# Kernel tuning notes

Measured on AMD Instinct MI355X. Metric: run time of the kernel, lower is better.

The kernel has to match this reference:

```python
import jax, jax.numpy as jnp
import numpy as np

B, C, H, W = 2, 64, 64, 128
HW = H * W
PCR = (0.0, -25.6, -3.0, 51.2, 25.6, 1.0)  # point cloud range x/y/z min, x/y/z max
VOX = (0.1, 0.1, 4.0)                      # voxel size
NX = int(round((PCR[3] - PCR[0]) / VOX[0]))  # 512
NY = int(round((PCR[4] - PCR[1]) / VOX[1]))  # 512
BIG = 1e10  # masked-out distance (avoid inf for clean vjp)


def _rand_points(key):
    k_xyz, k_i = jax.random.split(key)
    u = jax.random.uniform(k_xyz, (B, 3, H, W), jnp.float32)
    lo = jnp.array([PCR[0], PCR[1], PCR[2]], jnp.float32).reshape(1, 3, 1, 1)
    hi = jnp.array([PCR[3], PCR[4], PCR[5]], jnp.float32).reshape(1, 3, 1, 1)
    xyz = lo + u * (hi - lo)
    inten = jax.random.uniform(k_i, (B, 1, H, W), jnp.float32)
    return jnp.concatenate([xyz, inten], axis=1)  # (B,4,H,W)


def setup_inputs() -> dict:
    key = jax.random.key(0)
    k1, k2, k3, k4, k5 = jax.random.split(key, 5)
    return {
        "fv_features": jax.random.normal(k1, (B, C, H, W), jnp.float32),
        "points_img": _rand_points(k2),
        "proj_masks": jax.random.randint(k4, (B, H, W), 0, 2).astype(jnp.int32),
        "points_img_far": _rand_points(k3),
        "proj_masks_far": jax.random.randint(k5, (B, H, W), 0, 2).astype(jnp.int32),
    }


def _three_interpolate(near_pts, near_feats, near_valid, far_pts):
    """pointnet2 three_nn + three_interpolate with invalid near points masked.
    near_pts: (N,3), near_feats: (N,C), near_valid: (N,) bool, far_pts: (M,3).
    Returns interpolated far features (M,C)."""
    # squared distances via |a|^2 + |b|^2 - 2 a.b  -> (M, N), avoids (M,N,3) temp
    d2 = (jnp.sum(far_pts * far_pts, -1)[:, None]
          + jnp.sum(near_pts * near_pts, -1)[None, :]
          - 2.0 * far_pts @ near_pts.T)
    d2 = jnp.where(near_valid[None, :], d2, BIG)
    neg_d, idx = jax.lax.top_k(-d2, 3)        # 3 nearest near-points per far point
    dist = -neg_d                              # squared dists, as in pointnet2 CUDA
    dist_recip = 1.0 / (dist + 1e-8)
    weight = dist_recip / jnp.sum(dist_recip, axis=-1, keepdims=True)  # (M,3)
    gathered = near_feats[idx]                 # (M,3,C)
    return jnp.einsum('mk,mkc->mc', weight, gathered)


def _scatter_bev(pts, feats, valid):
    """Mean-scatter point features into the BEV grid. pts:(N,3) feats:(N,C) valid:(N,)."""
    ix = jnp.floor((pts[:, 0] - PCR[0]) / VOX[0]).astype(jnp.int32)
    iy = jnp.floor((pts[:, 1] - PCR[1]) / VOX[1]).astype(jnp.int32)
    in_range = (ix >= 0) & (ix < NX) & (iy >= 0) & (iy < NY)
    w = (valid & in_range).astype(feats.dtype)            # zero-weight invalid pts
    flat = jnp.clip(iy, 0, NY - 1) * NX + jnp.clip(ix, 0, NX - 1)
    sums = jnp.zeros((NY * NX, feats.shape[1]), feats.dtype).at[flat].add(feats * w[:, None])
    cnt = jnp.zeros((NY * NX,), feats.dtype).at[flat].add(w)
    bev = sums / jnp.maximum(cnt, 1.0)[:, None]
    return bev.reshape(NY, NX, -1).transpose(2, 0, 1)      # (C, NY, NX)


def reference(fv_features, points_img, proj_masks, points_img_far, proj_masks_far):
    feats = fv_features.transpose(0, 2, 3, 1).reshape(B, HW, C)
    pts = points_img[:, :3].transpose(0, 2, 3, 1).reshape(B, HW, 3)
    pts_far = points_img_far[:, :3].transpose(0, 2, 3, 1).reshape(B, HW, 3)
    m = proj_masks.reshape(B, HW) > 0
    m_far = proj_masks_far.reshape(B, HW) > 0
    outs = []
    for k in range(B):  # small fixed batch loop, mirrors original per-sample loop
        interp = _three_interpolate(pts[k], feats[k], m[k], pts_far[k])
        all_pts = jnp.concatenate([pts[k], pts_far[k]], axis=0)
        all_feats = jnp.concatenate([feats[k], interp], axis=0)
        all_valid = jnp.concatenate([m[k], m_far[k]], axis=0)
        outs.append(_scatter_bev(all_pts, all_feats, all_valid))
    return jnp.stack(outs, axis=0)  # (B, C, NY, NX)
```

## Files before the change

kernel.cpp:

```cpp
#include <hip/hip_runtime.h>
#include <math.h>

constexpr int B_  = 2;
constexpr int C_  = 64;
constexpr int HW_ = 64 * 128;
constexpr int N_  = HW_;
constexpr int NX_ = 512;
constexpr int NY_ = 512;
constexpr int NYNX_ = NX_ * NY_;
constexpr int GC_  = 32;
constexpr int GCC_ = GC_ * GC_;
constexpr int CAP_ = 48;
constexpr int LPF_ = 8;
constexpr int BN_  = B_ * N_;
constexpr int NNB_ = BN_ / (256 / LPF_);

__device__ __forceinline__ int voxel_of(float x, float y, float w) {
#pragma clang fp contract(off)
  if (w == 0.0f) return -1;
  float qx = (x - 0.0f) / 0.1f;
  float qy = (y - (-25.6f)) / 0.1f;
  int ix = (int)floorf(qx);
  int iy = (int)floorf(qy);
  if (ix < 0 || ix >= NX_ || iy < 0 || iy >= NY_) return -1;
  return iy * NX_ + ix;
}

__device__ __forceinline__ int gcell_x(float x) {
  int c = (int)floorf(x * 0.625f);
  return min(GC_ - 1, max(0, c));
}
__device__ __forceinline__ int gcell_y(float y) {
  int c = (int)floorf((y + 25.6f) * 0.625f);
  return min(GC_ - 1, max(0, c));
}

__global__ __launch_bounds__(256) void prep_kernel(
    const float* __restrict__ fv,
    const float* __restrict__ pi, const int* __restrict__ pm,
    const float* __restrict__ pif, const int* __restrict__ pmf,
    float4* __restrict__ near4, float4* __restrict__ far4,
    float* __restrict__ cnt, int* __restrict__ gcellcnt,
    float4* __restrict__ gpts, int* __restrict__ gidx,
    float* __restrict__ acc, float* __restrict__ fvT) {
#pragma clang fp contract(off)
  __shared__ float tile[64][65];
  if (blockIdx.x < 64) {
    int t = blockIdx.x * 256 + threadIdx.x;
    int k = t / N_, n = t % N_;
    const float* base  = pi  + (size_t)k * 4 * HW_;
    const float* basef = pif + (size_t)k * 4 * HW_;
    float x = base[n], y = base[HW_ + n], z = base[2 * HW_ + n];
    bool v = pm[k * HW_ + n] > 0;
    near4[t] = make_float4(x, y, z, v ? 1.0f : 0.0f);
    float fx = basef[n], fy = basef[HW_ + n], fz = basef[2 * HW_ + n];
    bool vf = pmf[k * HW_ + n] > 0;
    far4[t] = make_float4(fx, fy, fz, vf ? 1.0f : 0.0f);

    if (v) {
      float sq = (x * x + y * y) + z * z;
      int c = gcell_y(y) * GC_ + gcell_x(x);
      int p = atomicAdd(&gcellcnt[k * GCC_ + c], 1);
      if (p < CAP_) {
        size_t o = (size_t)(k * GCC_ + c) * CAP_ + p;
        gpts[o] = make_float4(x, y, z, sq);
        gidx[o] = n;
      }
    }

    float4 z4 = make_float4(0.0f, 0.0f, 0.0f, 0.0f);
    int vn = voxel_of(x, y, v ? 1.0f : 0.0f);
    if (vn >= 0) {
      float old = atomicAdd(&cnt[(size_t)k * NYNX_ + vn], 1.0f);
      if (old == 1.0f) {
        float4* row = (float4*)(acc + ((size_t)k * NYNX_ + vn) * C_);
#pragma unroll
        for (int i = 0; i < C_ / 4; ++i) row[i] = z4;
      }
    }
    int vfv = voxel_of(fx, fy, vf ? 1.0f : 0.0f);
    if (vfv >= 0) {
      float old2 = atomicAdd(&cnt[(size_t)k * NYNX_ + vfv], 1.0f);
      if (old2 == 1.0f) {
        float4* row = (float4*)(acc + ((size_t)k * NYNX_ + vfv) * C_);
#pragma unroll
        for (int i = 0; i < C_ / 4; ++i) row[i] = z4;
      }
    }
  } else {
    int bid = blockIdx.x - 64;
    int k = bid >> 7;
    int n0 = (bid & 127) * 64;
    int tx = threadIdx.x & 63, ty = threadIdx.x >> 6;
    for (int c = ty; c < C_; c += 4)
      tile[c][tx] = fv[((size_t)(k * C_ + c)) * HW_ + n0 + tx];
    __syncthreads();
    for (int nn = ty; nn < 64; nn += 4)
      fvT[((size_t)(k * HW_ + n0 + nn)) * C_ + tx] = tile[tx][nn];
  }
}

__device__ __forceinline__ void merge3L(float tv, int idx,
                                        float& b0, float& b1, float& b2,
                                        int& i0, int& i1, int& i2) {
  bool w0 = (tv < b0) || (tv == b0 && idx < i0);
  bool w1 = (tv < b1) || (tv == b1 && idx < i1);
  bool w2 = (tv < b2) || (tv == b2 && idx < i2);
  float ob0 = b0, ob1 = b1;
  int   oi0 = i0, oi1 = i1;
  b0 = w0 ? tv : b0;                    i0 = w0 ? idx : i0;
  b1 = w0 ? ob0 : (w1 ? tv : b1);       i1 = w0 ? oi0 : (w1 ? idx : i1);
  b2 = w1 ? ob1 : (w2 ? tv : b2);       i2 = w1 ? oi1 : (w2 ? idx : i2);
}

__global__ __launch_bounds__(256) void nn_scatter_kernel(
    const float4* __restrict__ far4, const int* __restrict__ gcellcnt,
    const float4* __restrict__ gpts, const int* __restrict__ gidx,
    const float4* __restrict__ near4, const float* __restrict__ fvT,
    const float* __restrict__ cnt, float* __restrict__ acc) {
#pragma clang fp contract(off)
  int tid = threadIdx.x;
  if (blockIdx.x < (unsigned)NNB_) {
    int q = tid & (LPF_ - 1);
    int g = blockIdx.x * (256 / LPF_) + (tid / LPF_);
    int k = g >> 13;
    int m = g & (N_ - 1);

    float4 f = far4[k * N_ + m];
    if (f.w == 0.0f) return;

    float sf = (f.x * f.x + f.y * f.y) + f.z * f.z;
    float ax = 2.0f * f.x, ay = 2.0f * f.y, az = 2.0f * f.z;
    int fcx = gcell_x(f.x), fcy = gcell_y(f.y);
    const int* gcc_ = gcellcnt + k * GCC_;

    float b0 = 1e30f, b1 = 1e30f, b2 = 1e30f;
    int i0 = 0, i1 = 0, i2 = 0;

    for (int r = 0; r < GC_; ++r) {
      int nc = (r == 0) ? 1 : 8 * r;
      for (int i = q; i < nc; i += LPF_) {
        int dx, dy;
        if (r == 0)            { dx = 0;             dy = 0; }
        else if (i < 2*r + 1)  { dx = i - r;         dy = -r; }
        else if (i < 4*r + 2)  { dx = i - (3*r + 1); dy = r; }
        else if (i < 6*r + 1)  { dx = -r;            dy = i - (5*r + 1); }
        else                   { dx = r;             dy = i - 7*r; }
        int cx = fcx + dx, cy = fcy + dy;
        if (cx < 0 || cx >= GC_ || cy < 0 || cy >= GC_) continue;
        int c = cy * GC_ + cx;
        int e = gcc_[c];
        if (e > CAP_) e = CAP_;
        const float4* gp = gpts + (size_t)(k * GCC_ + c) * CAP_;
        const int*    gi = gidx + (size_t)(k * GCC_ + c) * CAP_;
        for (int j = 0; j < e; ++j) {
          float4 p = gp[j];
          int idx = gi[j];
          float p0 = ax * p.x;
          float mm = __builtin_fmaf(az, p.z, __builtin_fmaf(ay, p.y, p0));
          float tv = (sf + p.w) - mm;
          merge3L(tv, idx, b0, b1, b2, i0, i1, i2);
        }
      }
      float s2 = b2;
      s2 = fminf(s2, __shfl_xor(s2, 1));
      s2 = fminf(s2, __shfl_xor(s2, 2));
      s2 = fminf(s2, __shfl_xor(s2, 4));
      float rd = (float)r * 1.6f;
      if (rd * rd > s2 + 0.01f) break;
    }

    int base = tid & ~(LPF_ - 1);
    for (int s = 1; s < LPF_; ++s) {
      float v0 = __shfl(b0, base + s), v1 = __shfl(b1, base + s), v2 = __shfl(b2, base + s);
      int   j0 = __shfl(i0, base + s), j1 = __shfl(i1, base + s), j2 = __shfl(i2, base + s);
      if (q == 0) {
        merge3L(v0, j0, b0, b1, b2, i0, i1, i2);
        merge3L(v1, j1, b0, b1, b2, i0, i1, i2);
        merge3L(v2, j2, b0, b1, b2, i0, i1, i2);
      }
    }
    float w0_ = 0.0f, w1_ = 0.0f, w2_ = 0.0f;
    if (q == 0) {
      float r0 = 1.0f / (b0 + 1e-8f);
      float r1 = 1.0f / (b1 + 1e-8f);
      float r2 = 1.0f / (b2 + 1e-8f);
      float rs = (r0 + r1) + r2;
      w0_ = r0 / rs; w1_ = r1 / rs; w2_ = r2 / rs;
    }
    float w0 = __shfl(w0_, base), w1 = __shfl(w1_, base), w2 = __shfl(w2_, base);
    int   j0 = __shfl(i0, base),  j1 = __shfl(i1, base),  j2 = __shfl(i2, base);

    int v = voxel_of(f.x, f.y, f.w);
    if (v < 0) return;
    float cn = cnt[(size_t)k * NYNX_ + v];
    const float4* r0p = (const float4*)(fvT + ((size_t)(k * N_ + j0)) * C_);
    const float4* r1p = (const float4*)(fvT + ((size_t)(k * N_ + j1)) * C_);
    const float4* r2p = (const float4*)(fvT + ((size_t)(k * N_ + j2)) * C_);
    size_t rowoff = ((size_t)k * NYNX_ + v) * C_;
#pragma unroll
    for (int h = 0; h < 2; ++h) {
      int c4 = q * 2 + h;
      float4 a = r0p[c4], b = r1p[c4], c = r2p[c4];
      float4 val;
      val.x = (w0 * a.x + w1 * b.x) + w2 * c.x;
      val.y = (w0 * a.y + w1 * b.y) + w2 * c.y;
      val.z = (w0 * a.z + w1 * b.z) + w2 * c.z;
      val.w = (w0 * a.w + w1 * b.w) + w2 * c.w;
      if (cn == 1.0f) {
        ((float4*)(acc + rowoff))[c4] = val;
      } else {
        float* p = acc + rowoff + c4 * 4;
        atomicAdd(p + 0, val.x); atomicAdd(p + 1, val.y);
        atomicAdd(p + 2, val.z); atomicAdd(p + 3, val.w);
      }
    }
  } else {
    int lane = tid & 63;
    int wv = (blockIdx.x - NNB_) * 4 + (tid >> 6);
    int k = wv >> 13;
    int n = wv & (N_ - 1);
    float4 pt = near4[k * N_ + n];
    int v = voxel_of(pt.x, pt.y, pt.w);
    if (v < 0) return;
    float val = fvT[((size_t)(k * N_ + n)) * C_ + lane];
    size_t rowoff = ((size_t)k * NYNX_ + v) * C_;
    float cn = cnt[(size_t)k * NYNX_ + v];
    if (cn == 1.0f) acc[rowoff + lane] = val;
    else            atomicAdd(&acc[rowoff + lane], val);
  }
}

__global__ __launch_bounds__(256) void emit_kernel(
    const float* __restrict__ acc, const float* __restrict__ cnt,
    float* __restrict__ out) {
#pragma clang fp contract(off)
  __shared__ float tile[64][65];
  __shared__ float cs[64];
  int t = threadIdx.x;
  int k = blockIdx.y;
  int v0 = blockIdx.x * 64;

  if (t < 64) cs[t] = cnt[(size_t)k * NYNX_ + v0 + t];
  __syncthreads();

  const float4* acc4 = (const float4*)acc;
#pragma unroll
  for (int p = 0; p < 4; ++p) {
    int row = p * 16 + (t >> 4);
    int f4  = t & 15;
    float c = cs[row];
    float4 a = make_float4(0.0f, 0.0f, 0.0f, 0.0f);
    if (c > 0.0f) {
      a = acc4[((size_t)k * NYNX_ + v0 + row) * (C_ / 4) + f4];
      a.x /= c; a.y /= c; a.z /= c; a.w /= c;
    }
    tile[f4 * 4 + 0][row] = a.x;
    tile[f4 * 4 + 1][row] = a.y;
    tile[f4 * 4 + 2][row] = a.z;
    tile[f4 * 4 + 3][row] = a.w;
  }
  __syncthreads();

#pragma unroll
  for (int p = 0; p < 4; ++p) {
    int c  = p * 16 + (t >> 4);
    int xq = t & 15;
    float4 o = make_float4(tile[c][xq * 4 + 0], tile[c][xq * 4 + 1],
                           tile[c][xq * 4 + 2], tile[c][xq * 4 + 3]);
    ((float4*)out)[(((size_t)k * C_ + c) * NYNX_ + v0) / 4 + xq] = o;
  }
}

extern "C" void kernel_launch(void* const* d_in, const int* in_sizes, int n_in,
                              void* d_out, int out_size, void* d_ws, size_t ws_size,
                              hipStream_t stream) {
  const float* fv  = (const float*)d_in[0];
  const float* pi  = (const float*)d_in[1];
  const int*   pm  = (const int*)d_in[2];
  const float* pif = (const float*)d_in[3];
  const int*   pmf = (const int*)d_in[4];
  float* out = (float*)d_out;

  char* wsb = (char*)d_ws;
  float*  fvT    = (float*)(wsb);
  float*  cnt    = (float*)(wsb + 4194304);
  int*    gcell  = (int*)(wsb + 6291456);
  float4* near4  = (float4*)(wsb + 6299648);
  float4* far4   = (float4*)(wsb + 6561792);
  float4* gpts   = (float4*)(wsb + 6823936);
  int*    gidx   = (int*)(wsb + 8396800);
  float*  acc    = (float*)(wsb + 16777216);

  hipMemsetAsync(cnt, 0, 2097152 + 8192, stream);

  prep_kernel<<<320, 256, 0, stream>>>(
      fv, pi, pm, pif, pmf, near4, far4, cnt, gcell, gpts, gidx, acc, fvT);
  nn_scatter_kernel<<<NNB_ + B_ * N_ / 4, 256, 0, stream>>>(
      far4, gcell, gpts, gidx, near4, fvT, cnt, acc);
  emit_kernel<<<dim3(NYNX_ / 64, B_), 256, 0, stream>>>(acc, cnt, out);
}
```

Before: 179.7 us.

## Compact BEV accumulator into dense slot array via wave-aggregated slot allocation

Result: slower. 185.6 us (+3.3%).

```diff
diff --git a/kernel.cpp b/kernel.cpp
--- a/kernel.cpp
+++ b/kernel.cpp
@@ -14,6 +14,8 @@
 constexpr int LPF_ = 8;
 constexpr int BN_  = B_ * N_;
 constexpr int NNB_ = BN_ / (256 / LPF_);
+constexpr int NSB_ = BN_ / 32;
+constexpr int MAXSLOT_ = 32768;
 
 __device__ __forceinline__ int voxel_of(float x, float y, float w) {
 #pragma clang fp contract(off)
@@ -35,14 +37,26 @@
   return min(GC_ - 1, max(0, c));
 }
 
+__device__ __forceinline__ int alloc_slot(int* nslot) {
+  unsigned long long mk = __ballot(1);
+  int lane = threadIdx.x & 63;
+  int lead = __ffsll((unsigned long long)mk) - 1;
+  int nact = __popcll(mk);
+  int basep = 0;
+  if (lane == lead) basep = atomicAdd(nslot, nact);
+  basep = __shfl(basep, lead);
+  return basep + __popcll(mk & ((1ull << lane) - 1ull));
+}
+
 __global__ __launch_bounds__(256) void prep_kernel(
     const float* __restrict__ fv,
     const float* __restrict__ pi, const int* __restrict__ pm,
     const float* __restrict__ pif, const int* __restrict__ pmf,
     float4* __restrict__ near4, float4* __restrict__ far4,
     float* __restrict__ cnt, int* __restrict__ gcellcnt,
+    int* __restrict__ nslot, int* __restrict__ slotmap,
     float4* __restrict__ gpts, int* __restrict__ gidx,
-    float* __restrict__ acc, float* __restrict__ fvT) {
+    float* __restrict__ fvT) {
 #pragma clang fp contract(off)
   __shared__ float tile[64][65];
   if (blockIdx.x < 64) {
@@ -68,24 +82,17 @@
       }
     }
 
-    float4 z4 = make_float4(0.0f, 0.0f, 0.0f, 0.0f);
     int vn = voxel_of(x, y, v ? 1.0f : 0.0f);
     if (vn >= 0) {
-      float old = atomicAdd(&cnt[(size_t)k * NYNX_ + vn], 1.0f);
-      if (old == 1.0f) {
-        float4* row = (float4*)(acc + ((size_t)k * NYNX_ + vn) * C_);
-#pragma unroll
-        for (int i = 0; i < C_ / 4; ++i) row[i] = z4;
-      }
+      int kv = k * NYNX_ + vn;
+      float old = atomicAdd(&cnt[kv], 1.0f);
+      if (old == 0.0f) slotmap[kv] = alloc_slot(nslot) + 1;
     }
     int vfv = voxel_of(fx, fy, vf ? 1.0f : 0.0f);
     if (vfv >= 0) {
-      float old2 = atomicAdd(&cnt[(size_t)k * NYNX_ + vfv], 1.0f);
-      if (old2 == 1.0f) {
-        float4* row = (float4*)(acc + ((size_t)k * NYNX_ + vfv) * C_);
-#pragma unroll
-        for (int i = 0; i < C_ / 4; ++i) row[i] = z4;
-      }
+      int kv = k * NYNX_ + vfv;
+      float old2 = atomicAdd(&cnt[kv], 1.0f);
+      if (old2 == 0.0f) slotmap[kv] = alloc_slot(nslot) + 1;
     }
   } else {
     int bid = blockIdx.x - 64;
@@ -117,7 +124,8 @@
     const float4* __restrict__ far4, const int* __restrict__ gcellcnt,
     const float4* __restrict__ gpts, const int* __restrict__ gidx,
     const float4* __restrict__ near4, const float* __restrict__ fvT,
-    const float* __restrict__ cnt, float* __restrict__ acc) {
+    const float* __restrict__ cnt, const int* __restrict__ slotmap,
+    float* __restrict__ acc) {
 #pragma clang fp contract(off)
   int tid = threadIdx.x;
   if (blockIdx.x < (unsigned)NNB_) {
@@ -193,11 +201,12 @@
 
     int v = voxel_of(f.x, f.y, f.w);
     if (v < 0) return;
-    float cn = cnt[(size_t)k * NYNX_ + v];
+    int kv = k * NYNX_ + v;
+    float cn = cnt[kv];
+    size_t rowoff = (size_t)(slotmap[kv] - 1) * C_;
     const float4* r0p = (const float4*)(fvT + ((size_t)(k * N_ + j0)) * C_);
     const float4* r1p = (const float4*)(fvT + ((size_t)(k * N_ + j1)) * C_);
     const float4* r2p = (const float4*)(fvT + ((size_t)(k * N_ + j2)) * C_);
-    size_t rowoff = ((size_t)k * NYNX_ + v) * C_;
 #pragma unroll
     for (int h = 0; h < 2; ++h) {
       int c4 = q * 2 + h;
@@ -216,32 +225,48 @@
       }
     }
   } else {
-    int lane = tid & 63;
-    int wv = (blockIdx.x - NNB_) * 4 + (tid >> 6);
-    int k = wv >> 13;
-    int n = wv & (N_ - 1);
+    int q = tid & 7;
+    int g = (blockIdx.x - NNB_) * 32 + (tid >> 3);
+    int k = g >> 13;
+    int n = g & (N_ - 1);
     float4 pt = near4[k * N_ + n];
+    if (pt.w == 0.0f) return;
     int v = voxel_of(pt.x, pt.y, pt.w);
     if (v < 0) return;
-    float val = fvT[((size_t)(k * N_ + n)) * C_ + lane];
-    size_t rowoff = ((size_t)k * NYNX_ + v) * C_;
-    float cn = cnt[(size_t)k * NYNX_ + v];
-    if (cn == 1.0f) acc[rowoff + lane] = val;
-    else            atomicAdd(&acc[rowoff + lane], val);
+    int kv = k * NYNX_ + v;
+    float cn = cnt[kv];
+    size_t rowoff = (size_t)(slotmap[kv] - 1) * C_;
+    const float4* src = (const float4*)(fvT + ((size_t)(k * N_ + n)) * C_);
+#pragma unroll
+    for (int h = 0; h < 2; ++h) {
+      int c4 = q * 2 + h;
+      float4 val = src[c4];
+      if (cn == 1.0f) {
+        ((float4*)(acc + rowoff))[c4] = val;
+      } else {
+        float* p = acc + rowoff + c4 * 4;
+        atomicAdd(p + 0, val.x); atomicAdd(p + 1, val.y);
+        atomicAdd(p + 2, val.z); atomicAdd(p + 3, val.w);
+      }
+    }
   }
 }
 
 __global__ __launch_bounds__(256) void emit_kernel(
     const float* __restrict__ acc, const float* __restrict__ cnt,
-    float* __restrict__ out) {
+    const int* __restrict__ slotmap, float* __restrict__ out) {
 #pragma clang fp contract(off)
   __shared__ float tile[64][65];
   __shared__ float cs[64];
+  __shared__ int   sl[64];
   int t = threadIdx.x;
   int k = blockIdx.y;
   int v0 = blockIdx.x * 64;
 
-  if (t < 64) cs[t] = cnt[(size_t)k * NYNX_ + v0 + t];
+  if (t < 64) {
+    cs[t] = cnt[(size_t)k * NYNX_ + v0 + t];
+    sl[t] = slotmap[(size_t)k * NYNX_ + v0 + t];
+  }
   __syncthreads();
 
   const float4* acc4 = (const float4*)acc;
@@ -252,7 +277,7 @@
     float c = cs[row];
     float4 a = make_float4(0.0f, 0.0f, 0.0f, 0.0f);
     if (c > 0.0f) {
-      a = acc4[((size_t)k * NYNX_ + v0 + row) * (C_ / 4) + f4];
+      a = acc4[(size_t)(sl[row] - 1) * (C_ / 4) + f4];
       a.x /= c; a.y /= c; a.z /= c; a.w /= c;
     }
     tile[f4 * 4 + 0][row] = a.x;
@@ -286,17 +311,20 @@
   float*  fvT    = (float*)(wsb);
   float*  cnt    = (float*)(wsb + 4194304);
   int*    gcell  = (int*)(wsb + 6291456);
-  float4* near4  = (float4*)(wsb + 6299648);
-  float4* far4   = (float4*)(wsb + 6561792);
-  float4* gpts   = (float4*)(wsb + 6823936);
-  int*    gidx   = (int*)(wsb + 8396800);
-  float*  acc    = (float*)(wsb + 16777216);
-
-  hipMemsetAsync(cnt, 0, 2097152 + 8192, stream);
+  int*    nslot  = (int*)(wsb + 6299648);
+  int*    slotmap= (int*)(wsb + 6299664);
+  float*  acc    = (float*)(wsb + 8396816);
+  float4* near4  = (float4*)(wsb + 16785424);
+  float4* far4   = (float4*)(wsb + 17047568);
+  float4* gpts   = (float4*)(wsb + 17309712);
+  int*    gidx   = (int*)(wsb + 18882576);
+
+  hipMemsetAsync(cnt, 0, 12591120, stream);
 
   prep_kernel<<<320, 256, 0, stream>>>(
-      fv, pi, pm, pif, pmf, near4, far4, cnt, gcell, gpts, gidx, acc, fvT);
-  nn_scatter_kernel<<<NNB_ + B_ * N_ / 4, 256, 0, stream>>>(
-      far4, gcell, gpts, gidx, near4, fvT, cnt, acc);
-  emit_kernel<<<dim3(NYNX_ / 64, B_), 256, 0, stream>>>(acc, cnt, out);
-}
+      fv, pi, pm, pif, pmf, near4, far4, cnt, gcell, nslot, slotmap,
+      gpts, gidx, fvT);
+  nn_scatter_kernel<<<NNB_ + NSB_, 256, 0, stream>>>(
+      far4, gcell, gpts, gidx, near4, fvT, cnt, slotmap, acc);
+  emit_kernel<<<dim3(NYNX_ / 64, B_), 256, 0, stream>>>(acc, cnt, slotmap, out);
+}
```
